# Kernel optimization log

Measured on AMD Instinct MI355X. Metric: run time of the kernel, lower is better.

Reference implementation:

```python
import jax, jax.numpy as jnp
import numpy as np

C = 64
G = 4
K = 3
GC = C // G
OS = 1.0  # offset_scale
OM_DIM = int(np.ceil(G * K * K * 3 / 8) * 8)  # 112, padded; only first G*27 used


def setup_inputs() -> dict:
    key = jax.random.key(0)
    ks = jax.random.split(key, 8)
    B, H, W = 2, 384, 384
    s = 0.02
    return {
        "inp": jax.random.normal(ks[0], (B, C, H, W), jnp.float32),
        "Wv": jax.random.normal(ks[1], (C, C), jnp.float32) * s,
        "bv": jnp.zeros((C,), jnp.float32),
        "Wdw": jax.random.normal(ks[2], (C, 1, K, K), jnp.float32) * s,
        "bdw": jnp.zeros((C,), jnp.float32),
        "Wom": jax.random.normal(ks[3], (C, OM_DIM), jnp.float32) * s,
        "bom": jnp.zeros((OM_DIM,), jnp.float32),
        "Wo": jax.random.normal(ks[4], (C, C), jnp.float32) * s,
    }


def _bilinear(v, px, py, H, W, b_idx, g_idx):
    # v: (B,H,W,G,GC); px,py: (B,H,W,G) pixel coords; zero padding outside.
    x0 = jnp.floor(px)
    y0 = jnp.floor(py)
    wx1 = px - x0
    wy1 = py - y0
    x0i = x0.astype(jnp.int32)
    y0i = y0.astype(jnp.int32)
    out = jnp.zeros(px.shape + (v.shape[-1],), v.dtype)
    for dy, wy in ((0, 1.0 - wy1), (1, wy1)):
        for dx, wx in ((0, 1.0 - wx1), (1, wx1)):
            xi = x0i + dx
            yi = y0i + dy
            valid = ((xi >= 0) & (xi < W) & (yi >= 0) & (yi < H)).astype(v.dtype)
            xc = jnp.clip(xi, 0, W - 1)
            yc = jnp.clip(yi, 0, H - 1)
            g = v[b_idx, yc, xc, g_idx]  # (B,H,W,G,GC)
            out = out + g * (wy * wx * valid)[..., None]
    return out


def reference(inp, Wv, bv, Wdw, bdw, Wom, bom, Wo):
    B, _, H, W = inp.shape
    x = inp.transpose(0, 2, 3, 1)  # (B,H,W,C)
    # value projection, split into groups
    value = (x @ Wv + bv).reshape(B, H, W, G, GC)
    # depthwise conv on input feeds the offset/mask predictor
    dw = jax.lax.conv_general_dilated(
        inp, Wdw, window_strides=(1, 1), padding=[(1, 1), (1, 1)],
        feature_group_count=C) + bdw[None, :, None, None]
    om = dw.transpose(0, 2, 3, 1) @ Wom + bom  # (B,H,W,OM_DIM)
    om = om[..., : G * K * K * 3].reshape(B, H, W, G, K * K * 3)
    off = om[..., : K * K * 2].reshape(B, H, W, G, K * K, 2)  # (dx,dy) per point
    mask = om[..., K * K * 2:]  # (B,H,W,G,K*K), no softmax in DCNv4

    base_x = jnp.arange(W, dtype=value.dtype)[None, None, :, None]
    base_y = jnp.arange(H, dtype=value.dtype)[None, :, None, None]
    b_idx = jnp.arange(B)[:, None, None, None]
    g_idx = jnp.arange(G)[None, None, None, :]

    out = jnp.zeros((B, H, W, G, GC), value.dtype)
    k = 0
    for ky in range(K):
        for kx in range(K):
            dx = off[..., k, 0]
            dy = off[..., k, 1]
            px = base_x + ((kx - K // 2) + dx) * OS
            py = base_y + ((ky - K // 2) + dy) * OS
            samp = _bilinear(value, px, py, H, W, b_idx, g_idx)
            out = out + samp * mask[..., k][..., None]
            k += 1

    out = out.reshape(B, H, W, C) @ Wo  # output_proj, no bias (output_bias=False)
    return out.transpose(0, 3, 1, 2)  # back to (B,C,H,W)
```

## Files before the change

### kernel.cpp

```cpp
#include <hip/hip_runtime.h>
#include <hip/hip_fp16.h>
#include <math.h>

namespace {
constexpr int kH = 384, kW = 384, kBn = 2;
constexpr int kHW = kH * kW;
constexpr int kOMD = 112;
constexpr int kNB = kBn * (kHW / 64);
constexpr int kNB8 = kNB / 8;
}

typedef _Float16 h2 __attribute__((ext_vector_type(2)));

__device__ unsigned g_Wom2[32 * kOMD];
__device__ unsigned g_Wo2[32 * 64];

__device__ __forceinline__ int swz(int t) {
    return (t & 7) * kNB8 + (t >> 3);
}

__device__ __forceinline__ unsigned pack2h(float a, float b) {
    unsigned short lo = __builtin_bit_cast(unsigned short, __float2half_rn(a));
    unsigned short hi = __builtin_bit_cast(unsigned short, __float2half_rn(b));
    return (unsigned)lo | ((unsigned)hi << 16);
}

#if __has_builtin(__builtin_amdgcn_fdot2)
__device__ __forceinline__ float dot2(unsigned a, unsigned b, float c) {
    return __builtin_amdgcn_fdot2(__builtin_bit_cast(h2, a),
                                  __builtin_bit_cast(h2, b), c, false);
}
#else
__device__ __forceinline__ float dot2(unsigned a, unsigned b, float c) {
    h2 ha = __builtin_bit_cast(h2, a), hb = __builtin_bit_cast(h2, b);
    c = fmaf((float)ha.x, (float)hb.x, c);
    c = fmaf((float)ha.y, (float)hb.y, c);
    return c;
}
#endif

__device__ __forceinline__ void acc8h(__half2* pa, const unsigned short* src,
                                      float wgt) {
    const uint4 u0 = ((const uint4*)src)[0];
    const uint4 u1 = ((const uint4*)src)[1];
    const __half2 w2 = __half2half2(__float2half_rn(wgt));
    pa[0] = __hfma2(w2, __builtin_bit_cast(__half2, u0.x), pa[0]);
    pa[1] = __hfma2(w2, __builtin_bit_cast(__half2, u0.y), pa[1]);
    pa[2] = __hfma2(w2, __builtin_bit_cast(__half2, u0.z), pa[2]);
    pa[3] = __hfma2(w2, __builtin_bit_cast(__half2, u0.w), pa[3]);
    pa[4] = __hfma2(w2, __builtin_bit_cast(__half2, u1.x), pa[4]);
    pa[5] = __hfma2(w2, __builtin_bit_cast(__half2, u1.y), pa[5]);
    pa[6] = __hfma2(w2, __builtin_bit_cast(__half2, u1.z), pa[6]);
    pa[7] = __hfma2(w2, __builtin_bit_cast(__half2, u1.w), pa[7]);
}

__global__ __launch_bounds__(256) void k_value(
        const float* __restrict__ inp, const float* __restrict__ Wv,
        const float* __restrict__ bv, const float* __restrict__ Wom,
        const float* __restrict__ Wo, unsigned short* __restrict__ value) {
    __shared__ float xin[64][64];
    const int tid = threadIdx.x;

    if (blockIdx.x == 0) {
        for (int i = tid; i < 32 * kOMD; i += 256) {
            const int ci2 = i / kOMD, j = i % kOMD;
            g_Wom2[i] = pack2h(Wom[(2 * ci2) * kOMD + j],
                               Wom[(2 * ci2 + 1) * kOMD + j]);
        }
        for (int i = tid; i < 32 * 64; i += 256) {
            const int ci2 = i >> 6, j = i & 63;
            g_Wo2[i] = pack2h(Wo[(2 * ci2) * 64 + j],
                              Wo[(2 * ci2 + 1) * 64 + j]);
        }
    }

    const int bid = swz(blockIdx.x);
    const int b = bid / (kHW / 64);
    const int pix0 = (bid % (kHW / 64)) * 64;
    const float* ib = inp + (size_t)b * 64 * kHW + pix0;
    for (int i = tid; i < 1024; i += 256) {
        const int c = i >> 4, p4 = (i & 15) << 2;
        const float4 v = *(const float4*)(ib + (size_t)c * kHW + p4);
        *(float4*)&xin[c][p4] = v;
    }
    __syncthreads();

    const int p = tid & 63;
    const int gs = __builtin_amdgcn_readfirstlane(tid >> 6);

    float acc[16];
    {
        const float* bg = bv + gs * 16;
        #pragma unroll
        for (int j = 0; j < 16; ++j) acc[j] = bg[j];
    }
    #pragma unroll 4
    for (int ci = 0; ci < 64; ++ci) {
        const float a = xin[ci][p];
        const float* wr = Wv + ci * 64 + gs * 16;
        #pragma unroll
        for (int j = 0; j < 16; ++j) acc[j] = fmaf(a, wr[j], acc[j]);
    }

    unsigned u[8];
    #pragma unroll
    for (int j = 0; j < 8; ++j) u[j] = pack2h(acc[2 * j], acc[2 * j + 1]);
    uint4* vo = (uint4*)(value + ((size_t)(b * 4 + gs) * kHW + pix0 + p) * 16);
    vo[0] = make_uint4(u[0], u[1], u[2], u[3]);
    vo[1] = make_uint4(u[4], u[5], u[6], u[7]);
}

__global__ __launch_bounds__(256) void k_main(
        const float* __restrict__ inp, const float* __restrict__ Wdw,
        const float* __restrict__ bdw, const float* __restrict__ bom,
        const unsigned short* __restrict__ value, float* __restrict__ out) {
    __shared__ unsigned lds2[32][64];

    const int tid = threadIdx.x;
    const int bid = swz(blockIdx.x);
    const int b = bid / (kH * (kW / 64));
    const int rem = bid % (kH * (kW / 64));
    const int h = rem / (kW / 64);
    const int w0 = (rem % (kW / 64)) * 64;

    const int p = tid & 63;
    const int gs = __builtin_amdgcn_readfirstlane(tid >> 6);

    {
        const int w = w0 + p;
        #pragma unroll 2
        for (int q = 0; q < 8; ++q) {
            float sv[2];
            #pragma unroll
            for (int e = 0; e < 2; ++e) {
                const int c = gs * 16 + 2 * q + e;
                const float* ib = inp + (size_t)(b * 64 + c) * kHW;
                float s = bdw[c];
                #pragma unroll
                for (int r = 0; r < 3; ++r) {
                    const int y = h - 1 + r;
                    if (y >= 0 && y < kH) {
                        const float* rowp = ib + (size_t)y * kW;
                        #pragma unroll
                        for (int kx = 0; kx < 3; ++kx) {
                            const int x = w - 1 + kx;
                            const float v = (x >= 0 && x < kW) ? rowp[x] : 0.f;
                            s = fmaf(v, Wdw[c * 9 + r * 3 + kx], s);
                        }
                    }
                }
                sv[e] = s;
            }
            lds2[gs * 8 + q][p] = pack2h(sv[0], sv[1]);
        }
    }
    __syncthreads();

    float om[27];
    {
        const float* bg = bom + gs * 27;
        #pragma unroll
        for (int j = 0; j < 27; ++j) om[j] = bg[j];
        #pragma unroll 4
        for (int ci2 = 0; ci2 < 32; ++ci2) {
            const unsigned a2 = lds2[ci2][p];
            const unsigned* wr = g_Wom2 + ci2 * kOMD + gs * 27;
            #pragma unroll
            for (int j = 0; j < 27; ++j) om[j] = dot2(a2, wr[j], om[j]);
        }
    }
    __syncthreads();

    {
        __half2 pa[8];
        #pragma unroll
        for (int j = 0; j < 8; ++j) pa[j] = __builtin_bit_cast(__half2, 0u);
        const float fw = (float)(w0 + p);
        const float fh = (float)h;
        const unsigned short* vbase = value + (size_t)(b * 4 + gs) * kHW * 16;
        #pragma unroll
        for (int k = 0; k < 9; ++k) {
            const int ky = k / 3, kx = k % 3;
            const float dx = om[2 * k];
            const float dy = om[2 * k + 1];
            const float m = om[18 + k];
            const float px = fw + (float)(kx - 1) + dx;
            const float py = fh + (float)(ky - 1) + dy;
            const float x0f = floorf(px), y0f = floorf(py);
            const int x0 = (int)x0f, y0 = (int)y0f;
            const float wx1 = px - x0f, wy1 = py - y0f;
            const float wx0 = 1.f - wx1, wy0 = 1.f - wy1;
            const bool interior = (x0 >= 0) & (y0 >= 0) &
                                  (x0 < kW - 1) & (y0 < kH - 1);
            if (__all(interior)) {
                const unsigned short* b00 = vbase + ((size_t)y0 * kW + x0) * 16;
                const float wy0m = wy0 * m, wy1m = wy1 * m;
                acc8h(pa, b00,                wx0 * wy0m);
                acc8h(pa, b00 + 16,           wx1 * wy0m);
                acc8h(pa, b00 + kW * 16,      wx0 * wy1m);
                acc8h(pa, b00 + kW * 16 + 16, wx1 * wy1m);
            } else {
                #pragma unroll
                for (int cor = 0; cor < 4; ++cor) {
                    const int dy2 = cor >> 1, dx2 = cor & 1;
                    const int xi = x0 + dx2, yi = y0 + dy2;
                    float wgt = (dy2 ? wy1 : wy0) * (dx2 ? wx1 : wx0) * m;
                    if (xi < 0 || xi >= kW || yi < 0 || yi >= kH) wgt = 0.f;
                    const int xc = min(max(xi, 0), kW - 1);
                    const int yc = min(max(yi, 0), kH - 1);
                    acc8h(pa, vbase + ((size_t)yc * kW + xc) * 16, wgt);
                }
            }
        }
        #pragma unroll
        for (int j = 0; j < 8; ++j)
            lds2[gs * 8 + j][p] = __builtin_bit_cast(unsigned, pa[j]);
    }
    __syncthreads();

    {
        float acc[16];
        #pragma unroll
        for (int j = 0; j < 16; ++j) acc[j] = 0.f;
        #pragma unroll 4
        for (int ci2 = 0; ci2 < 32; ++ci2) {
            const unsigned a2 = lds2[ci2][p];
            const unsigned* wr = g_Wo2 + ci2 * 64 + gs * 16;
            #pragma unroll
            for (int j = 0; j < 16; ++j) acc[j] = dot2(a2, wr[j], acc[j]);
        }
        float* ob = out + (size_t)(b * 64 + gs * 16) * kHW + (size_t)h * kW + w0 + p;
        #pragma unroll
        for (int j = 0; j < 16; ++j) ob[(size_t)j * kHW] = acc[j];
    }
}

extern "C" void kernel_launch(void* const* d_in, const int* in_sizes, int n_in,
                              void* d_out, int out_size, void* d_ws, size_t ws_size,
                              hipStream_t stream) {
    const float* inp = (const float*)d_in[0];
    const float* Wv  = (const float*)d_in[1];
    const float* bv  = (const float*)d_in[2];
    const float* Wdw = (const float*)d_in[3];
    const float* bdw = (const float*)d_in[4];
    const float* Wom = (const float*)d_in[5];
    const float* bom = (const float*)d_in[6];
    const float* Wo  = (const float*)d_in[7];
    float* outp = (float*)d_out;
    unsigned short* value = (unsigned short*)d_ws;

    k_value<<<kNB, 256, 0, stream>>>(inp, Wv, bv, Wom, Wo, value);
    k_main<<<kNB, 256, 0, stream>>>(inp, Wdw, bdw, bom, value, outp);
}
```

Before: 306.3 us.

## Compute value projection with split-fp16 MFMA and separate weight prep kernel

Measured after the change: 306.7 us. No clear change (+0.1%).

```diff
diff --git a/kernel.cpp b/kernel.cpp
--- a/kernel.cpp
+++ b/kernel.cpp
@@ -11,9 +11,13 @@
 }
 
 typedef _Float16 h2 __attribute__((ext_vector_type(2)));
+typedef _Float16 half8 __attribute__((ext_vector_type(8)));
+typedef float f32x4 __attribute__((ext_vector_type(4)));
 
 __device__ unsigned g_Wom2[32 * kOMD];
 __device__ unsigned g_Wo2[32 * 64];
+__device__ __align__(16) _Float16 g_WvFh[4 * 2 * 64 * 8];
+__device__ __align__(16) _Float16 g_WvFl[4 * 2 * 64 * 8];
 
 __device__ __forceinline__ int swz(int t) {
     return (t & 7) * kNB8 + (t >> 3);
@@ -23,6 +27,12 @@
     unsigned short lo = __builtin_bit_cast(unsigned short, __float2half_rn(a));
     unsigned short hi = __builtin_bit_cast(unsigned short, __float2half_rn(b));
     return (unsigned)lo | ((unsigned)hi << 16);
+}
+
+__device__ __forceinline__ unsigned packhh(_Float16 a, _Float16 b) {
+    const unsigned short ua = __builtin_bit_cast(unsigned short, a);
+    const unsigned short ub = __builtin_bit_cast(unsigned short, b);
+    return (unsigned)ua | ((unsigned)ub << 16);
 }
 
 #if __has_builtin(__builtin_amdgcn_fdot2)
@@ -54,60 +64,102 @@
     pa[7] = __hfma2(w2, __builtin_bit_cast(__half2, u1.w), pa[7]);
 }
 
+__device__ __forceinline__ half8 ld_frag_g(const _Float16* ptr) {
+    return __builtin_bit_cast(half8, *(const uint4*)ptr);
+}
+
+__global__ __launch_bounds__(256) void k_prep(
+        const float* __restrict__ Wv, const float* __restrict__ Wom,
+        const float* __restrict__ Wo) {
+    const int tid = threadIdx.x;
+    for (int i = tid; i < 4 * 2 * 64 * 8; i += 256) {
+        const int jj = i & 7, l = (i >> 3) & 63, kh = (i >> 9) & 1, mt = i >> 10;
+        const int co = mt * 16 + (l & 15);
+        const int ch = kh * 32 + ((l >> 4) & 3) * 8 + jj;
+        const float w = Wv[ch * 64 + co];
+        const _Float16 hi = (_Float16)w;
+        g_WvFh[i] = hi;
+        g_WvFl[i] = (_Float16)((w - (float)hi) * 2048.f);
+    }
+    for (int i = tid; i < 32 * kOMD; i += 256) {
+        const int ci2 = i / kOMD, j = i % kOMD;
+        g_Wom2[i] = pack2h(Wom[(2 * ci2) * kOMD + j],
+                           Wom[(2 * ci2 + 1) * kOMD + j]);
+    }
+    for (int i = tid; i < 32 * 64; i += 256) {
+        const int ci2 = i >> 6, j = i & 63;
+        g_Wo2[i] = pack2h(Wo[(2 * ci2) * 64 + j],
+                          Wo[(2 * ci2 + 1) * 64 + j]);
+    }
+}
+
 __global__ __launch_bounds__(256) void k_value(
-        const float* __restrict__ inp, const float* __restrict__ Wv,
-        const float* __restrict__ bv, const float* __restrict__ Wom,
-        const float* __restrict__ Wo, unsigned short* __restrict__ value) {
-    __shared__ float xin[64][64];
+        const float* __restrict__ inp, const float* __restrict__ bv,
+        unsigned short* __restrict__ value) {
+    __shared__ unsigned xh[8][64][4];
+    __shared__ unsigned xl[8][64][4];
     const int tid = threadIdx.x;
-
-    if (blockIdx.x == 0) {
-        for (int i = tid; i < 32 * kOMD; i += 256) {
-            const int ci2 = i / kOMD, j = i % kOMD;
-            g_Wom2[i] = pack2h(Wom[(2 * ci2) * kOMD + j],
-                               Wom[(2 * ci2 + 1) * kOMD + j]);
-        }
-        for (int i = tid; i < 32 * 64; i += 256) {
-            const int ci2 = i >> 6, j = i & 63;
-            g_Wo2[i] = pack2h(Wo[(2 * ci2) * 64 + j],
-                              Wo[(2 * ci2 + 1) * 64 + j]);
-        }
-    }
-
     const int bid = swz(blockIdx.x);
     const int b = bid / (kHW / 64);
     const int pix0 = (bid % (kHW / 64)) * 64;
     const float* ib = inp + (size_t)b * 64 * kHW + pix0;
-    for (int i = tid; i < 1024; i += 256) {
-        const int c = i >> 4, p4 = (i & 15) << 2;
-        const float4 v = *(const float4*)(ib + (size_t)c * kHW + p4);
-        *(float4*)&xin[c][p4] = v;
+
+    #pragma unroll
+    for (int it = 0; it < 2; ++it) {
+        const int i = tid + it * 256;
+        const int c8 = i >> 6, px = i & 63;
+        const float* src = ib + (size_t)(c8 * 8) * kHW + px;
+        unsigned uh[4], ul[4];
+        #pragma unroll
+        for (int e = 0; e < 4; ++e) {
+            const float x0 = src[(size_t)(2 * e) * kHW];
+            const float x1 = src[(size_t)(2 * e + 1) * kHW];
+            const _Float16 h0 = (_Float16)x0, h1 = (_Float16)x1;
+            const _Float16 l0 = (_Float16)((x0 - (float)h0) * 2048.f);
+            const _Float16 l1 = (_Float16)((x1 - (float)h1) * 2048.f);
+            uh[e] = packhh(h0, h1);
+            ul[e] = packhh(l0, l1);
+        }
+        *(uint4*)&xh[c8][px][0] = make_uint4(uh[0], uh[1], uh[2], uh[3]);
+        *(uint4*)&xl[c8][px][0] = make_uint4(ul[0], ul[1], ul[2], ul[3]);
     }
     __syncthreads();
 
-    const int p = tid & 63;
-    const int gs = __builtin_amdgcn_readfirstlane(tid >> 6);
-
-    float acc[16];
-    {
-        const float* bg = bv + gs * 16;
-        #pragma unroll
-        for (int j = 0; j < 16; ++j) acc[j] = bg[j];
-    }
-    #pragma unroll 4
-    for (int ci = 0; ci < 64; ++ci) {
-        const float a = xin[ci][p];
-        const float* wr = Wv + ci * 64 + gs * 16;
-        #pragma unroll
-        for (int j = 0; j < 16; ++j) acc[j] = fmaf(a, wr[j], acc[j]);
-    }
-
-    unsigned u[8];
+    const int l = tid & 63;
+    const int wv = __builtin_amdgcn_readfirstlane(tid >> 6);
+    const int lr = l & 15, q = l >> 4;
+    const int px = wv * 16 + lr;
+
+    half8 bhf[2], blf[2];
     #pragma unroll
-    for (int j = 0; j < 8; ++j) u[j] = pack2h(acc[2 * j], acc[2 * j + 1]);
-    uint4* vo = (uint4*)(value + ((size_t)(b * 4 + gs) * kHW + pix0 + p) * 16);
-    vo[0] = make_uint4(u[0], u[1], u[2], u[3]);
-    vo[1] = make_uint4(u[4], u[5], u[6], u[7]);
+    for (int kh = 0; kh < 2; ++kh) {
+        bhf[kh] = __builtin_bit_cast(half8, *(const uint4*)&xh[kh * 4 + q][px][0]);
+        blf[kh] = __builtin_bit_cast(half8, *(const uint4*)&xl[kh * 4 + q][px][0]);
+    }
+    #pragma unroll
+    for (int mt = 0; mt < 4; ++mt) {
+        const half8 ah0 = ld_frag_g(g_WvFh + ((mt * 2 + 0) * 64 + l) * 8);
+        const half8 ah1 = ld_frag_g(g_WvFh + ((mt * 2 + 1) * 64 + l) * 8);
+        const half8 al0 = ld_frag_g(g_WvFl + ((mt * 2 + 0) * 64 + l) * 8);
+        const half8 al1 = ld_frag_g(g_WvFl + ((mt * 2 + 1) * 64 + l) * 8);
+        f32x4 acc = {0.f, 0.f, 0.f, 0.f};
+        f32x4 acc2 = {0.f, 0.f, 0.f, 0.f};
+        acc  = __builtin_amdgcn_mfma_f32_16x16x32_f16(ah0, bhf[0], acc, 0, 0, 0);
+        acc  = __builtin_amdgcn_mfma_f32_16x16x32_f16(ah1, bhf[1], acc, 0, 0, 0);
+        acc2 = __builtin_amdgcn_mfma_f32_16x16x32_f16(ah0, blf[0], acc2, 0, 0, 0);
+        acc2 = __builtin_amdgcn_mfma_f32_16x16x32_f16(ah1, blf[1], acc2, 0, 0, 0);
+        acc2 = __builtin_amdgcn_mfma_f32_16x16x32_f16(al0, bhf[0], acc2, 0, 0, 0);
+        acc2 = __builtin_amdgcn_mfma_f32_16x16x32_f16(al1, bhf[1], acc2, 0, 0, 0);
+        const float4 b4 = *(const float4*)(bv + mt * 16 + q * 4);
+        const float v0 = acc[0] + acc2[0] * (1.f / 2048.f) + b4.x;
+        const float v1 = acc[1] + acc2[1] * (1.f / 2048.f) + b4.y;
+        const float v2 = acc[2] + acc2[2] * (1.f / 2048.f) + b4.z;
+        const float v3 = acc[3] + acc2[3] * (1.f / 2048.f) + b4.w;
+        uint2 st;
+        st.x = pack2h(v0, v1);
+        st.y = pack2h(v2, v3);
+        *(uint2*)(value + ((size_t)(b * 4 + mt) * kHW + pix0 + px) * 16 + q * 4) = st;
+    }
 }
 
 __global__ __launch_bounds__(256) void k_main(
@@ -249,6 +301,7 @@
     float* outp = (float*)d_out;
     unsigned short* value = (unsigned short*)d_ws;
 
-    k_value<<<kNB, 256, 0, stream>>>(inp, Wv, bv, Wom, Wo, value);
+    k_prep<<<1, 256, 0, stream>>>(Wv, Wom, Wo);
+    k_value<<<kNB, 256, 0, stream>>>(inp, bv, value);
     k_main<<<kNB, 256, 0, stream>>>(inp, Wdw, bdw, bom, value, outp);
 }
```
